# Kernel optimization log

Measured on AMD Instinct MI355X. Metric: run time of the kernel, lower is better.

The kernel has to match this reference:

```python
import jax, jax.numpy as jnp
import numpy as np

B, H, W = 12, 192, 640
EPS = 1e-7
THRESHOLD = 0.98


def _normalize_flow(f):
    # torch: 2*(f - min)/(max - min) - 1 with GLOBAL min/max
    mn = f.min()
    mx = f.max()
    return 2.0 * (f - mn) / (mx - mn) - 1.0


def setup_inputs() -> dict:
    key = jax.random.key(0)
    ks = jax.random.split(key, 4)
    # optical flow in pixels (up to ~tens of px displacement)
    flow = jax.random.normal(ks[0], (B, 2, H, W), jnp.float32) * 20.0
    depth = jax.random.uniform(ks[1], (B, 1, H, W), jnp.float32, minval=0.1, maxval=10.0)
    # realistic pinhole intrinsics (KITTI-like), padded to 4x4
    Kn = np.eye(4, dtype=np.float32)
    Kn[0, 0] = 0.58 * W
    Kn[1, 1] = 1.92 * H
    Kn[0, 2] = 0.5 * W
    Kn[1, 2] = 0.5 * H
    K = jnp.tile(jnp.asarray(Kn)[None], (B, 1, 1))
    invK = jnp.tile(jnp.asarray(np.linalg.inv(Kn))[None], (B, 1, 1))
    # small-motion camera pose: identity rotation + small translation
    t = jax.random.normal(ks[2], (B, 3), jnp.float32) * 0.05
    pose = jnp.tile(jnp.eye(4, dtype=jnp.float32)[None], (B, 1, 1)).at[:, :3, 3].set(t)
    segmentation = jax.random.randint(ks[3], (B, 1, H, W), 0, 2) > 0
    return {"flow": flow, "depth": depth, "K": K, "invK": invK,
            "pose": pose, "segmentation": segmentation}


def reference(flow, depth, K, invK, pose, segmentation):
    gx = jnp.arange(W, dtype=jnp.float32)
    gy = jnp.arange(H, dtype=jnp.float32)
    grid = jnp.stack(jnp.meshgrid(gx, gy, indexing='xy'), axis=0)  # [2,H,W]

    # ---- compute_dynamic_flow: BackprojectDepth + Project3D + normalize + mask ----
    flow_n = _normalize_flow(flow)
    pix = jnp.concatenate([grid.reshape(2, -1),
                           jnp.ones((1, H * W), jnp.float32)], axis=0)  # [3,HW]
    cam = jnp.einsum('bij,jn->bin', invK[:, :3, :3], pix)               # [B,3,HW]
    cam = depth.reshape(B, 1, -1) * cam
    points = jnp.concatenate([cam, jnp.ones((B, 1, H * W), cam.dtype)], axis=1)  # [B,4,HW]
    P = jnp.matmul(K, pose)[:, :3, :]                                   # [B,3,4]
    cp = jnp.einsum('bij,bjn->bin', P, points)                          # [B,3,HW]
    pix_locs = (cp[:, :2] / (cp[:, 2:3] + EPS)).reshape(B, 2, H, W)
    static_n = _normalize_flow(pix_locs - grid[None])
    dyn = flow_n - static_n
    check = jnp.sqrt(jnp.sum(dyn * dyn, axis=1, keepdims=True))         # [B,1,H,W]
    check = (check - check.min()) / (check.max() - check.min())
    motion_mask = check < THRESHOLD

    coords = jnp.round(grid[None] + flow).astype(jnp.int32)             # [B,2,H,W]
    cxi = jnp.clip(coords[:, 0], 0, W - 1)
    cyi = jnp.clip(coords[:, 1], 0, H - 1)
    idx = (cyi * W + cxi).reshape(B, -1)                                # [B,HW]

    def scat(idx_b, vals_b):  # vals_b: [C,HW] -> scatter columns to idx_b
        return jnp.zeros_like(vals_b).at[:, idx_b].set(vals_b)

    bwd_flow = jax.vmap(scat)(idx, (-flow).reshape(B, 2, -1)).reshape(B, 2, H, W)
    seg_ref = jax.vmap(scat)(idx, segmentation.reshape(B, 1, -1)).reshape(B, 1, H, W)

    return motion_mask, bwd_flow, seg_ref
```

## Files before the change

kernel.cpp:

```cpp
#include <hip/hip_runtime.h>
#include <math.h>

#pragma clang fp contract(off)

namespace {

constexpr int B = 12, H = 192, W = 640;
constexpr int HW  = H * W;
constexpr int BHW = B * HW;
constexpr int NQ  = BHW / 4;
constexpr float EPS = 1e-7f;

constexpr int TA  = 256;
constexpr int GA  = NQ / TA;
constexpr int BPB = (HW / 4) / TA;

constexpr int TR    = 6;
constexpr int TILES = H / TR;
constexpr int TRW   = TR * W;
constexpr int NBK   = B * TILES;
constexpr int GW    = NBK;
constexpr int GC    = 416;
constexpr int CGRID = GW + GC;
constexpr int TPB   = 1024;


__device__ __forceinline__ void computeP(const float* __restrict__ Kb,
                                         const float* __restrict__ Po, float* P) {
#pragma unroll
    for (int i = 0; i < 3; ++i)
#pragma unroll
        for (int j = 0; j < 4; ++j) {
            float s = Kb[i*4+0] * Po[0*4+j];
            s = s + Kb[i*4+1] * Po[1*4+j];
            s = s + Kb[i*4+2] * Po[2*4+j];
            s = s + Kb[i*4+3] * Po[3*4+j];
            P[i*4+j] = s;
        }
}

__device__ __forceinline__ void static_flow_P(
    const float* __restrict__ iK, const float* __restrict__ P,
    int x, int y, float d, float& sx, float& sy)
{
    float fx = (float)x, fy = (float)y;
    float cam0 = iK[0]*fx + iK[1]*fy + iK[2];
    float cam1 = iK[4]*fx + iK[5]*fy + iK[6];
    float cam2 = iK[8]*fx + iK[9]*fy + iK[10];
    cam0 = d * cam0; cam1 = d * cam1; cam2 = d * cam2;
    float cp0 = P[0]*cam0 + P[1]*cam1 + P[2]*cam2  + P[3];
    float cp1 = P[4]*cam0 + P[5]*cam1 + P[6]*cam2  + P[7];
    float cp2 = P[8]*cam0 + P[9]*cam1 + P[10]*cam2 + P[11];
    float pz = cp2 + EPS;
    sx = cp0 / pz - fx;
    sy = cp1 / pz - fy;
}

__device__ __forceinline__ float norm01(float v, float mn, float mx) {
    return (2.0f * (v - mn)) / (mx - mn) - 1.0f;
}

template<int NW>
__device__ __forceinline__ void blockRed4T(float& a0, float& a1, float& a2, float& a3,
                                           float (*sred)[4], float* bc) {
    for (int off = 32; off; off >>= 1) {
        a0 = fminf(a0, __shfl_down(a0, off, 64));
        a1 = fmaxf(a1, __shfl_down(a1, off, 64));
        a2 = fminf(a2, __shfl_down(a2, off, 64));
        a3 = fmaxf(a3, __shfl_down(a3, off, 64));
    }
    int lane = threadIdx.x & 63, wv = threadIdx.x >> 6;
    if (lane == 0) { sred[wv][0]=a0; sred[wv][1]=a1; sred[wv][2]=a2; sred[wv][3]=a3; }
    __syncthreads();
    if (threadIdx.x == 0) {
#pragma unroll
        for (int w = 1; w < NW; ++w) {
            a0 = fminf(a0, sred[w][0]); a1 = fmaxf(a1, sred[w][1]);
            a2 = fminf(a2, sred[w][2]); a3 = fmaxf(a3, sred[w][3]);
        }
        bc[0]=a0; bc[1]=a1; bc[2]=a2; bc[3]=a3;
    }
    __syncthreads();
    a0=bc[0]; a1=bc[1]; a2=bc[2]; a3=bc[3];
}

template<int NW>
__device__ __forceinline__ void blockRed2T(float& a0, float& a1,
                                           float (*sred)[4], float* bc) {
    for (int off = 32; off; off >>= 1) {
        a0 = fminf(a0, __shfl_down(a0, off, 64));
        a1 = fmaxf(a1, __shfl_down(a1, off, 64));
    }
    int lane = threadIdx.x & 63, wv = threadIdx.x >> 6;
    if (lane == 0) { sred[wv][0]=a0; sred[wv][1]=a1; }
    __syncthreads();
    if (threadIdx.x == 0) {
#pragma unroll
        for (int w = 1; w < NW; ++w) {
            a0 = fminf(a0, sred[w][0]); a1 = fmaxf(a1, sred[w][1]);
        }
        bc[0]=a0; bc[1]=a1;
    }
    __syncthreads();
    a0=bc[0]; a1=bc[1];
}

__global__ void kZ(unsigned* __restrict__ cnt) {
    cnt[threadIdx.x] = 0u;
}

__global__ void __launch_bounds__(TA)
kA(const float* __restrict__ flow, const float* __restrict__ depth,
   const float* __restrict__ Km, const float* __restrict__ invK,
   const float* __restrict__ pose,
   unsigned* __restrict__ cnt, unsigned* __restrict__ bkt,
   float* __restrict__ redA)
{
    __shared__ float sred[4][4];
    __shared__ float bc[4];
    __shared__ unsigned tcnt[TILES];
    __shared__ unsigned tbase[TILES];

    if (threadIdx.x < TILES) tcnt[threadIdx.x] = 0u;
    __syncthreads();

    int g  = blockIdx.x * TA + threadIdx.x;
    int p0 = g * 4;
    int b  = p0 / HW;
    float P[12];
    computeP(Km + b*16, pose + b*16, P);
    const float* iK = invK + b * 16;
    int n0 = p0 - b * HW;
    int y  = n0 / W;
    int x0 = n0 - y * W;
    float4 fx4 = *(const float4*)(flow + b*2*HW + n0);
    float4 fy4 = *(const float4*)(flow + b*2*HW + HW + n0);
    float4 d4  = *(const float4*)(depth + p0);
    float fmn = fminf(fminf(fx4.x, fx4.y), fminf(fx4.z, fx4.w));
    float fmx = fmaxf(fmaxf(fx4.x, fx4.y), fmaxf(fx4.z, fx4.w));
    fmn = fminf(fmn, fminf(fminf(fy4.x, fy4.y), fminf(fy4.z, fy4.w)));
    fmx = fmaxf(fmx, fmaxf(fmaxf(fy4.x, fy4.y), fmaxf(fy4.z, fy4.w)));
    float smn = INFINITY, smx = -INFINITY;
    float fxa[4] = {fx4.x, fx4.y, fx4.z, fx4.w};
    float fya[4] = {fy4.x, fy4.y, fy4.z, fy4.w};
    float da[4]  = {d4.x, d4.y, d4.z, d4.w};
    int      t_j[4];
    unsigned off_j[4], e_j[4];
#pragma unroll
    for (int j = 0; j < 4; ++j) {
        float sx, sy;
        static_flow_P(iK, P, x0 + j, y, da[j], sx, sy);
        smn = fminf(smn, fminf(sx, sy));
        smx = fmaxf(smx, fmaxf(sx, sy));
        int cxi = (int)rintf((float)(x0 + j) + fxa[j]);
        int cyi = (int)rintf((float)y + fya[j]);
        cxi = min(max(cxi, 0), W - 1);
        cyi = min(max(cyi, 0), H - 1);
        int t   = cyi / TR;
        int pos = (cyi - t * TR) * W + cxi;
        t_j[j]   = t;
        e_j[j]   = ((unsigned)(n0 + j) << 12) | (unsigned)pos;
        off_j[j] = atomicAdd(&tcnt[t], 1u);
    }
    __syncthreads();
    if (threadIdx.x < TILES)
        tbase[threadIdx.x] =
            atomicAdd(&cnt[b * TILES + threadIdx.x], tcnt[threadIdx.x]);
    __syncthreads();
#pragma unroll
    for (int j = 0; j < 4; ++j) {
        int idx = (b * TILES + t_j[j]) * HW + (int)(tbase[t_j[j]] + off_j[j]);
        bkt[idx] = e_j[j];
    }

    blockRed4T<4>(fmn, fmx, smn, smx, sred, bc);
    if (threadIdx.x == 0) {
        redA[blockIdx.x*4+0] = fmn; redA[blockIdx.x*4+1] = fmx;
        redA[blockIdx.x*4+2] = smn; redA[blockIdx.x*4+3] = smx;
    }
}

__global__ void __launch_bounds__(TPB)
kBW(const float* __restrict__ flow, const float* __restrict__ depth,
    const float* __restrict__ Km, const float* __restrict__ invK,
    const float* __restrict__ pose, const int* __restrict__ seg,
    const unsigned* __restrict__ cnt, const unsigned* __restrict__ bkt,
    const float* __restrict__ redA, float* __restrict__ redB,
    float* __restrict__ out)
{
    __shared__ unsigned smem[TRW];
    if (blockIdx.x < GW) {
        const int wb = blockIdx.x;
        const int b  = wb / TILES;
        const int t  = wb - b * TILES;
        for (int i = threadIdx.x; i < TRW; i += TPB) smem[i] = 0u;
        __syncthreads();

        const unsigned count = cnt[wb];
        const unsigned* src = bkt + wb * HW;
        for (unsigned i = threadIdx.x; i < count; i += TPB) {
            unsigned e = src[i];
            atomicMax(&smem[e & 4095u], (e >> 12) + 1u);
        }
        __syncthreads();

        const float* fb = flow + b * 2 * HW;
        const int*   sb = seg + b * HW;
        const int    nbase = t * TRW;
        for (int q = threadIdx.x; q < TRW/4; q += TPB) {
            uint4 w4 = *(const uint4*)(smem + q*4);
            unsigned wa[4] = {w4.x, w4.y, w4.z, w4.w};
            float4 bx4, by4, sg4;
            float* bxa = (float*)&bx4;
            float* bya = (float*)&by4;
            float* sga = (float*)&sg4;
#pragma unroll
            for (int j = 0; j < 4; ++j) {
                float bx = 0.0f, by = 0.0f, sg = 0.0f;
                if (wa[j]) {
                    int nw = (int)wa[j] - 1;
                    bx = -fb[nw];
                    by = -fb[HW + nw];
                    sg = sb[nw] ? 1.0f : 0.0f;
                }
                bxa[j] = bx; bya[j] = by; sga[j] = sg;
            }
            int n = nbase + q * 4;
            *(float4*)(out + BHW + b*2*HW + n)      = bx4;
            *(float4*)(out + BHW + b*2*HW + HW + n) = by4;
            *(float4*)(out + 3*BHW + b*HW + n)      = sg4;
        }
        return;
    }

    float (*sred)[4] = (float(*)[4])smem;
    float* bc = (float*)(smem + 64);

    float gfmn = INFINITY, gfmx = -INFINITY, gsmn = INFINITY, gsmx = -INFINITY;
    for (int i = threadIdx.x; i < GA; i += TPB) {
        gfmn = fminf(gfmn, redA[i*4+0]); gfmx = fmaxf(gfmx, redA[i*4+1]);
        gsmn = fminf(gsmn, redA[i*4+2]); gsmx = fmaxf(gsmx, redA[i*4+3]);
    }
    blockRed4T<16>(gfmn, gfmx, gsmn, gsmx, sred, bc);

    float cmn = INFINITY, cmx = -INFINITY;
    float P[12]; int bCur = -1;
    const int cb = blockIdx.x - GW;
    const int stride = GC * TPB;
    for (int g = cb * TPB + threadIdx.x; g < NQ; g += stride) {
        int p0 = g * 4;
        int b  = p0 / HW;
        if (b != bCur) { computeP(Km + b*16, pose + b*16, P); bCur = b; }
        const float* iK = invK + b * 16;
        int n0 = p0 - b * HW;
        int y  = n0 / W;
        int x0 = n0 - y * W;
        float4 fx4 = *(const float4*)(flow + b*2*HW + n0);
        float4 fy4 = *(const float4*)(flow + b*2*HW + HW + n0);
        float4 d4  = *(const float4*)(depth + p0);
        float fxa[4] = {fx4.x, fx4.y, fx4.z, fx4.w};
        float fya[4] = {fy4.x, fy4.y, fy4.z, fy4.w};
        float da[4]  = {d4.x, d4.y, d4.z, d4.w};
        float4 cv;
        float* cva = (float*)&cv;
#pragma unroll
        for (int j = 0; j < 4; ++j) {
            float sx, sy;
            static_flow_P(iK, P, x0 + j, y, da[j], sx, sy);
            float dx = norm01(fxa[j], gfmn, gfmx) - norm01(sx, gsmn, gsmx);
            float dy = norm01(fya[j], gfmn, gfmx) - norm01(sy, gsmn, gsmx);
            float c = sqrtf(dx*dx + dy*dy);
            cva[j] = c;
            cmn = fminf(cmn, c); cmx = fmaxf(cmx, c);
        }
        *(float4*)(out + p0) = cv;
    }
    blockRed2T<16>(cmn, cmx, sred, bc);
    if (threadIdx.x == 0) { redB[cb*2] = cmn; redB[cb*2+1] = cmx; }
}

__global__ void __launch_bounds__(TA)
kM(const float* __restrict__ redB, float* __restrict__ out)
{
    __shared__ float sred[4][4];
    __shared__ float bc[4];

    float gcmn = INFINITY, gcmx = -INFINITY;
    for (int i = threadIdx.x; i < GC; i += TA) {
        gcmn = fminf(gcmn, redB[2*i]); gcmx = fmaxf(gcmx, redB[2*i+1]);
    }
    blockRed2T<4>(gcmn, gcmx, sred, bc);

    int p0 = (blockIdx.x * TA + threadIdx.x) * 4;
    float4 c4 = *(const float4*)(out + p0);
    float ca[4] = {c4.x, c4.y, c4.z, c4.w};
    float4 m4;
    float* ma = (float*)&m4;
#pragma unroll
    for (int j = 0; j < 4; ++j) {
        float cn = (ca[j] - gcmn) / (gcmx - gcmn);
        ma[j] = (cn < 0.98f) ? 1.0f : 0.0f;
    }
    *(float4*)(out + p0) = m4;
}

}

extern "C" void kernel_launch(void* const* d_in, const int* in_sizes, int n_in,
                              void* d_out, int out_size, void* d_ws, size_t ws_size,
                              hipStream_t stream) {
    const float* flow  = (const float*)d_in[0];
    const float* depth = (const float*)d_in[1];
    const float* Km    = (const float*)d_in[2];
    const float* invK  = (const float*)d_in[3];
    const float* pose  = (const float*)d_in[4];
    const int*   seg   = (const int*)d_in[5];
    float* out = (float*)d_out;

    unsigned* cnt  = (unsigned*)d_ws;
    float*    redA = (float*)((char*)d_ws + 4096);
    float*    redB = (float*)((char*)d_ws + 28672);
    unsigned* bkt  = (unsigned*)((char*)d_ws + 32768);

    kZ <<<1,     NBK, 0, stream>>>(cnt);
    kA <<<GA,    TA,  0, stream>>>(flow, depth, Km, invK, pose, cnt, bkt, redA);
    kBW<<<CGRID, TPB, 0, stream>>>(flow, depth, Km, invK, pose, seg, cnt, bkt,
                                   redA, redB, out);
    kM <<<GA,    TA,  0, stream>>>(redB, out);
}
```

Before: 137.4 us.

## Use per-block fixed-capacity bucket segments, pack segmentation bit, drop zeroing kernel

Kernel kA no longer takes global atomicAdd offsets into per-tile buckets. Each block writes its entries into a private fixed-capacity segment per tile and records its counts, which removes the global atomics, a barrier, and the separate zeroing kernel launch. The segmentation bit is packed into the bucket entry, so the scatter kernel no longer does a gathered read of seg. The scatter kernel now walks per-block segments one wavefront at a time and remaps block indices across XCDs for locality. The trade-off is a larger, sparser workspace and more loop overhead in the consumer.

```diff
diff --git a/kernel.cpp b/kernel.cpp
--- a/kernel.cpp
+++ b/kernel.cpp
@@ -23,6 +23,7 @@
 constexpr int GC    = 416;
 constexpr int CGRID = GW + GC;
 constexpr int TPB   = 1024;
+constexpr int SEGCAP = 1024;
 
 
 __device__ __forceinline__ void computeP(const float* __restrict__ Kb,
@@ -105,28 +106,23 @@
     a0=bc[0]; a1=bc[1];
 }
 
-__global__ void kZ(unsigned* __restrict__ cnt) {
-    cnt[threadIdx.x] = 0u;
-}
-
 __global__ void __launch_bounds__(TA)
 kA(const float* __restrict__ flow, const float* __restrict__ depth,
    const float* __restrict__ Km, const float* __restrict__ invK,
-   const float* __restrict__ pose,
-   unsigned* __restrict__ cnt, unsigned* __restrict__ bkt,
+   const float* __restrict__ pose, const int* __restrict__ seg,
+   unsigned* __restrict__ cntA, unsigned* __restrict__ bkt,
    float* __restrict__ redA)
 {
     __shared__ float sred[4][4];
     __shared__ float bc[4];
     __shared__ unsigned tcnt[TILES];
-    __shared__ unsigned tbase[TILES];
 
     if (threadIdx.x < TILES) tcnt[threadIdx.x] = 0u;
     __syncthreads();
 
-    int g  = blockIdx.x * TA + threadIdx.x;
-    int p0 = g * 4;
-    int b  = p0 / HW;
+    int p0 = blockIdx.x * (TA * 4) + threadIdx.x * 4;
+    int b  = blockIdx.x / BPB;
+    int blkInB = blockIdx.x - b * BPB;
     float P[12];
     computeP(Km + b*16, pose + b*16, P);
     const float* iK = invK + b * 16;
@@ -136,6 +132,7 @@
     float4 fx4 = *(const float4*)(flow + b*2*HW + n0);
     float4 fy4 = *(const float4*)(flow + b*2*HW + HW + n0);
     float4 d4  = *(const float4*)(depth + p0);
+    int4   s4  = *(const int4*)(seg + p0);
     float fmn = fminf(fminf(fx4.x, fx4.y), fminf(fx4.z, fx4.w));
     float fmx = fmaxf(fmaxf(fx4.x, fx4.y), fmaxf(fx4.z, fx4.w));
     fmn = fminf(fmn, fminf(fminf(fy4.x, fy4.y), fminf(fy4.z, fy4.w)));
@@ -144,8 +141,9 @@
     float fxa[4] = {fx4.x, fx4.y, fx4.z, fx4.w};
     float fya[4] = {fy4.x, fy4.y, fy4.z, fy4.w};
     float da[4]  = {d4.x, d4.y, d4.z, d4.w};
+    int   sa[4]  = {s4.x, s4.y, s4.z, s4.w};
     int      t_j[4];
-    unsigned off_j[4], e_j[4];
+    unsigned r_j[4], e_j[4];
 #pragma unroll
     for (int j = 0; j < 4; ++j) {
         float sx, sy;
@@ -158,19 +156,18 @@
         cyi = min(max(cyi, 0), H - 1);
         int t   = cyi / TR;
         int pos = (cyi - t * TR) * W + cxi;
-        t_j[j]   = t;
-        e_j[j]   = ((unsigned)(n0 + j) << 12) | (unsigned)pos;
-        off_j[j] = atomicAdd(&tcnt[t], 1u);
+        unsigned ns = ((unsigned)(n0 + j) << 1) | (sa[j] ? 1u : 0u);
+        t_j[j] = t;
+        e_j[j] = (ns << 12) | (unsigned)pos;
+        r_j[j] = atomicAdd(&tcnt[t], 1u);
     }
     __syncthreads();
     if (threadIdx.x < TILES)
-        tbase[threadIdx.x] =
-            atomicAdd(&cnt[b * TILES + threadIdx.x], tcnt[threadIdx.x]);
-    __syncthreads();
+        cntA[blockIdx.x * TILES + threadIdx.x] = tcnt[threadIdx.x];
 #pragma unroll
     for (int j = 0; j < 4; ++j) {
-        int idx = (b * TILES + t_j[j]) * HW + (int)(tbase[t_j[j]] + off_j[j]);
-        bkt[idx] = e_j[j];
+        size_t base = ((size_t)((b * TILES + t_j[j]) * BPB + blkInB)) * SEGCAP;
+        bkt[base + r_j[j]] = e_j[j];
     }
 
     blockRed4T<4>(fmn, fmx, smn, smx, sred, bc);
@@ -183,29 +180,35 @@
 __global__ void __launch_bounds__(TPB)
 kBW(const float* __restrict__ flow, const float* __restrict__ depth,
     const float* __restrict__ Km, const float* __restrict__ invK,
-    const float* __restrict__ pose, const int* __restrict__ seg,
-    const unsigned* __restrict__ cnt, const unsigned* __restrict__ bkt,
+    const float* __restrict__ pose,
+    const unsigned* __restrict__ cntA, const unsigned* __restrict__ bkt,
     const float* __restrict__ redA, float* __restrict__ redB,
     float* __restrict__ out)
 {
     __shared__ unsigned smem[TRW];
     if (blockIdx.x < GW) {
-        const int wb = blockIdx.x;
-        const int b  = wb / TILES;
-        const int t  = wb - b * TILES;
+        const int xcd = blockIdx.x & 7;
+        const int k   = blockIdx.x >> 3;
+        const int wp  = xcd * 48 + k;
+        const int b   = wp >> 5;
+        const int t   = wp & 31;
+
         for (int i = threadIdx.x; i < TRW; i += TPB) smem[i] = 0u;
         __syncthreads();
 
-        const unsigned count = cnt[wb];
-        const unsigned* src = bkt + wb * HW;
-        for (unsigned i = threadIdx.x; i < count; i += TPB) {
-            unsigned e = src[i];
-            atomicMax(&smem[e & 4095u], (e >> 12) + 1u);
+        const int wv = threadIdx.x >> 6, lane = threadIdx.x & 63;
+        for (int s = wv; s < BPB; s += 16) {
+            unsigned c = cntA[(b * BPB + s) * TILES + t];
+            const unsigned* src =
+                bkt + ((size_t)((b * TILES + t) * BPB + s)) * SEGCAP;
+            for (unsigned i = lane; i < c; i += 64) {
+                unsigned e = src[i];
+                atomicMax(&smem[e & 4095u], (e >> 12) + 1u);
+            }
         }
         __syncthreads();
 
         const float* fb = flow + b * 2 * HW;
-        const int*   sb = seg + b * HW;
         const int    nbase = t * TRW;
         for (int q = threadIdx.x; q < TRW/4; q += TPB) {
             uint4 w4 = *(const uint4*)(smem + q*4);
@@ -218,10 +221,11 @@
             for (int j = 0; j < 4; ++j) {
                 float bx = 0.0f, by = 0.0f, sg = 0.0f;
                 if (wa[j]) {
-                    int nw = (int)wa[j] - 1;
+                    unsigned u = wa[j] - 1u;
+                    int nw = (int)(u >> 1);
+                    sg = (u & 1u) ? 1.0f : 0.0f;
                     bx = -fb[nw];
                     by = -fb[HW + nw];
-                    sg = sb[nw] ? 1.0f : 0.0f;
                 }
                 bxa[j] = bx; bya[j] = by; sga[j] = sg;
             }
@@ -317,14 +321,14 @@
     const int*   seg   = (const int*)d_in[5];
     float* out = (float*)d_out;
 
-    unsigned* cnt  = (unsigned*)d_ws;
-    float*    redA = (float*)((char*)d_ws + 4096);
-    float*    redB = (float*)((char*)d_ws + 28672);
-    unsigned* bkt  = (unsigned*)((char*)d_ws + 32768);
-
-    kZ <<<1,     NBK, 0, stream>>>(cnt);
-    kA <<<GA,    TA,  0, stream>>>(flow, depth, Km, invK, pose, cnt, bkt, redA);
-    kBW<<<CGRID, TPB, 0, stream>>>(flow, depth, Km, invK, pose, seg, cnt, bkt,
-                                   redA, redB, out);
+    float*    redA = (float*)d_ws;
+    float*    redB = (float*)((char*)d_ws + 24576);
+    unsigned* cntA = (unsigned*)((char*)d_ws + 32768);
+    unsigned* bkt  = (unsigned*)((char*)d_ws + 262144);
+
+    kA <<<GA,    TA,  0, stream>>>(flow, depth, Km, invK, pose, seg,
+                                   cntA, bkt, redA);
+    kBW<<<CGRID, TPB, 0, stream>>>(flow, depth, Km, invK, pose,
+                                   cntA, bkt, redA, redB, out);
     kM <<<GA,    TA,  0, stream>>>(redB, out);
 }
```

Result: faster. 120.2 us (-12.5%).
